# Kernel optimization log

Measured on AMD Instinct MI355X. Metric: run time of the kernel, lower is better.

Reference implementation:

```python
import jax, jax.numpy as jnp
import numpy as np

MAX_LEN, BATCH, EMB = 512, 32, 41
HID, UNITS = 800, 20
BOND_LENS = jnp.array([1.329, 1.459, 1.525], jnp.float32)
BOND_ANGLES = jnp.array([2.034, 2.119, 1.937], jnp.float32)
INIT_ABC = jnp.array([[0.0, 0.0, 1.0], [0.0, 1.0, 0.0], [1.0, 0.0, 0.0]], jnp.float32)


def _lstm_dir(x, w_ih, w_hh, b, reverse):
    # x: [T, B, in]; returns hidden states [T, B, H]
    T, B, _ = x.shape
    H = w_hh.shape[1]
    xs = jnp.flip(x, 0) if reverse else x
    xw = jnp.einsum('tbi,gi->tbg', xs, w_ih) + b  # precompute input projection

    def step(carry, xt):
        h, c = carry
        gates = xt + h @ w_hh.T
        i, f, g, o = jnp.split(gates, 4, axis=-1)
        c = jax.nn.sigmoid(f) * c + jax.nn.sigmoid(i) * jnp.tanh(g)
        h = jax.nn.sigmoid(o) * jnp.tanh(c)
        return (h, c), h

    init = (jnp.zeros((B, H), x.dtype), jnp.zeros((B, H), x.dtype))
    _, hs = jax.lax.scan(step, init, xw)
    return jnp.flip(hs, 0) if reverse else hs


def _bilstm_layer(x, w_ih, w_hh, b):
    # w_ih: [2, 4H, in]; w_hh: [2, 4H, H]; b: [2, 4H]
    fwd = _lstm_dir(x, w_ih[0], w_hh[0], b[0], False)
    bwd = _lstm_dir(x, w_ih[1], w_hh[1], b[1], True)
    return jnp.concatenate([fwd, bwd], axis=-1)


def _geometric_unit(coords3, triplet):
    # coords3: [3, B, 3] last three atoms; triplet: [B, 3] torsion angles
    A, Bc, C = coords3[0], coords3[1], coords3[2]
    new = []
    for i in range(3):
        Tang, R, P = BOND_ANGLES[i], BOND_LENS[i], triplet[:, i]
        D2 = jnp.stack([-R * jnp.cos(Tang) * jnp.ones_like(P),
                        R * jnp.cos(P) * jnp.sin(Tang),
                        R * jnp.sin(P) * jnp.sin(Tang)], axis=1)  # [B,3]
        BC = C - Bc
        bc = BC / jnp.linalg.norm(BC, axis=1, keepdims=True)
        AB = Bc - A
        N = jnp.cross(AB, bc)
        n = N / jnp.linalg.norm(N, axis=1, keepdims=True)
        M = jnp.stack([bc, jnp.cross(n, bc), n], axis=2)  # [B,3,3]
        D = jnp.einsum('bij,bj->bi', M, D2) + C
        A, Bc, C = Bc, C, D
        new.append(D)
    return jnp.stack([A, Bc, C]), jnp.stack(new)  # carry, [3,B,3]


def setup_inputs() -> dict:
    key = jax.random.key(0)
    ks = jax.random.split(key, 10)
    k = 1.0 / np.sqrt(HID)
    u = lambda kk, shp, lim: jax.random.uniform(kk, shp, jnp.float32, -lim, lim)
    in0, in1 = EMB + 1, 2 * HID
    return {
        'sequences': jax.random.normal(ks[0], (MAX_LEN, BATCH, EMB), jnp.float32),
        'lengths': jnp.full((BATCH,), MAX_LEN, jnp.int64 if jax.config.jax_enable_x64 else jnp.int32),
        'w_ih0': u(ks[1], (2, 4 * HID, in0), k),
        'w_hh0': u(ks[2], (2, 4 * HID, HID), k),
        'b0': u(ks[3], (2, 4 * HID), k),
        'w_ih1': u(ks[4], (2, 4 * HID, in1), k),
        'w_hh1': u(ks[5], (2, 4 * HID, HID), k),
        'b1': u(ks[6], (2, 4 * HID), k),
        'lin_w': u(ks[7], (UNITS, 2 * HID), 1.0 / np.sqrt(2 * HID)),
        'lin_b': u(ks[8], (UNITS,), 1.0 / np.sqrt(2 * HID)),
        'alphabet': jax.random.uniform(ks[9], (UNITS, 3), jnp.float32, -3.14, 3.14),
    }


def reference(sequences, lengths, w_ih0, w_hh0, b0, w_ih1, w_hh1, b1, lin_w, lin_b, alphabet):
    T, B, _ = sequences.shape
    abs_pos = jnp.broadcast_to(jnp.arange(T, dtype=sequences.dtype)[:, None, None], (T, B, 1))
    x = jnp.concatenate([sequences, abs_pos], axis=2)  # [T, B, EMB+1]
    # 2-layer bidirectional LSTM (all lengths == max_len -> packing is identity)
    h = _bilstm_layer(x, w_ih0, w_hh0, b0)
    h = _bilstm_layer(h, w_ih1, w_hh1, b1)  # [T, B, 2H]
    # linear -> softmax over alphabet, trig angle decode
    soft = jax.nn.softmax(h @ lin_w.T + lin_b, axis=2)  # [T, B, UNITS]
    sine = soft @ jnp.sin(alphabet)   # [T, B, 3]
    cosine = soft @ jnp.cos(alphabet)
    out = jnp.arctan2(sine, cosine)   # torsion angle triplets
    # sequential geometric coordinate recurrence over timesteps 1..T-1
    init = jnp.broadcast_to(INIT_ABC[:, None, :], (3, B, 3))
    _, new_coords = jax.lax.scan(_geometric_unit, init, out[1:])  # [T-1, 3, B, 3]
    pred_coords = jnp.concatenate([init, new_coords.reshape(-1, B, 3)], axis=0)
    return pred_coords  # [3 + 3*(T-1), B, 3]
```

## Files before the change

kernel.cpp:

```cpp
#include <hip/hip_runtime.h>
#include <math.h>

#define T_LEN 512
#define NB    32
#define EMB_  41
#define IN0_  42
#define HID_  800
#define G4_   3200
#define IN1_  1600
#define NU    20
#define NCH0  50
#define NCH   100

typedef unsigned short u16;
typedef unsigned int   u32;
typedef unsigned long long u64;
typedef __attribute__((ext_vector_type(8))) short short8;
typedef __attribute__((ext_vector_type(4))) float f32x4;

__device__ __forceinline__ float bf2f(u16 v) {
    union { u32 u; float f; } c; c.u = ((u32)v) << 16; return c.f;
}
__device__ __forceinline__ u16 f2bf(float f) {
    union { float f; u32 u; } c; c.f = f;
    u32 r = (c.u + 0x7fffu + ((c.u >> 16) & 1u)) >> 16;
    return (u16)r;
}
__device__ __forceinline__ short cvt_hl(float v, int hl) {
    u16 hi = f2bf(v);
    return hl ? (short)f2bf(v - bf2f(hi)) : (short)hi;
}
__device__ __forceinline__ f32x4 mfma16(short8 a, short8 b, f32x4 c) {
    return __builtin_amdgcn_mfma_f32_16x16x32_bf16(a, b, c, 0, 0, 0);
}
__device__ __forceinline__ void astore(u64* p, u64 v) {
    __hip_atomic_store(p, v, __ATOMIC_RELAXED, __HIP_MEMORY_SCOPE_AGENT);
}
__device__ __forceinline__ int afload(const int* p) {
    return __hip_atomic_load(p, __ATOMIC_RELAXED, __HIP_MEMORY_SCOPE_AGENT);
}
__device__ __forceinline__ void afstore(int* p, int v) {
    __hip_atomic_store(p, v, __ATOMIC_RELAXED, __HIP_MEMORY_SCOPE_AGENT);
}


__global__ __launch_bounds__(256, 1)
void lstm0_persist(const float* __restrict__ seq, const float* __restrict__ wih0,
                   const float* __restrict__ whh0, const float* __restrict__ bias,
                   u16* __restrict__ h0f, int* __restrict__ flags)
{
    __shared__ __align__(16) float part[4096];
    __shared__ __align__(16) u16 stageB[25600];
    __shared__ __align__(16) float w0l[64*48];
    __shared__ __align__(16) float xsl[2][32*48];
    __shared__ u16 hpk[2][NB*8];
    const int tid = threadIdx.x;
    const int d = blockIdx.x / NCH0, ch = blockIdx.x % NCH0;
    const int w = tid >> 6, l = tid & 63;
    const int p = w & 1, hl = w >> 1;
    int* myflags = flags + d*128;

    short8 wreg[2][25];
    {
        const int m = l & 15, g = p*2 + (m>>3);
#pragma unroll
        for (int T = 0; T < 2; ++T) {
            const int j = (ch*2 + T)*8 + (m&7);
            const float* base = whh0 + ((size_t)(d*G4_ + g*HID_ + j))*HID_ + (l>>4)*8;
#pragma unroll
            for (int kc = 0; kc < 25; ++kc) {
                float4 f0 = *(const float4*)(base + kc*32);
                float4 f1 = *(const float4*)(base + kc*32 + 4);
                short8 v;
                v[0]=cvt_hl(f0.x,hl); v[1]=cvt_hl(f0.y,hl); v[2]=cvt_hl(f0.z,hl); v[3]=cvt_hl(f0.w,hl);
                v[4]=cvt_hl(f1.x,hl); v[5]=cvt_hl(f1.y,hl); v[6]=cvt_hl(f1.z,hl); v[7]=cvt_hl(f1.w,hl);
                wreg[T][kc] = v;
            }
        }
    }
    for (int idx = tid; idx < 64*EMB_; idx += 256) {
        int r = idx / EMB_, k = idx % EMB_;
        int ju_ = r >> 2, g = r & 3;
        w0l[r*48 + k] = wih0[((size_t)(d*G4_ + g*HID_ + ch*16 + ju_))*IN0_ + k];
    }
    const int ju = tid >> 5, b = tid & 31;
    const int nt = b >> 4, n = b & 15;
    float biasr[2][4], wpos[2][4];
#pragma unroll
    for (int T = 0; T < 2; ++T) {
        const int j = ch*16 + T*8 + ju;
#pragma unroll
        for (int g = 0; g < 4; ++g) {
            biasr[T][g] = bias[d*G4_ + g*HID_ + j];
            wpos[T][g]  = wih0[((size_t)(d*G4_ + g*HID_ + j))*IN0_ + EMB_];
        }
    }
    float creg[2] = {0.f, 0.f};
    __syncthreads();

    for (int s = 0; s < T_LEN; ++s) {
        const int t = d ? (T_LEN-1-s) : s;

        for (int idx = tid; idx < 32*EMB_; idx += 256)
            xsl[s&1][(idx/EMB_)*48 + idx%EMB_] = seq[(size_t)t*(NB*EMB_) + idx];

        if (s > 0 && tid < NCH0)
            while (afload(myflags + tid) < s) __builtin_amdgcn_s_sleep(1);
        __syncthreads();

        if (s == 0) {
#pragma unroll
            for (int q = 0; q < 25; ++q) ((u64*)stageB)[tid + q*256] = 0ull;
        } else {
            const int tprev = d ? (T_LEN - s) : (s - 1);
            const u64* src = (const u64*)(h0f + (size_t)tprev*51200) + d*6400;
            u64 tmp[25];
#pragma unroll
            for (int q = 0; q < 25; ++q) tmp[q] = src[tid + q*256];
#pragma unroll
            for (int q = 0; q < 25; ++q) ((u64*)stageB)[tid + q*256] = tmp[q];
        }
        __syncthreads();

        f32x4 a00 = {0.f,0.f,0.f,0.f}, a01 = {0.f,0.f,0.f,0.f};
        f32x4 a10 = {0.f,0.f,0.f,0.f}, a11 = {0.f,0.f,0.f,0.f};
#pragma unroll
        for (int kc = 0; kc < 25; ++kc) {
            short8 b0 = *(const short8*)(stageB + kc*1024 + l*8);
            short8 b1 = *(const short8*)(stageB + kc*1024 + 512 + l*8);
            a00 = mfma16(wreg[0][kc], b0, a00);
            a01 = mfma16(wreg[0][kc], b1, a01);
            a10 = mfma16(wreg[1][kc], b0, a10);
            a11 = mfma16(wreg[1][kc], b1, a11);
        }
        {
            const int mrow = (l>>4)*4, nn = l & 15;
#pragma unroll
            for (int r = 0; r < 4; ++r) {
                part[((0*8 + (p*2+hl)*2 + 0)*16 + mrow + r)*16 + nn] = a00[r];
                part[((0*8 + (p*2+hl)*2 + 1)*16 + mrow + r)*16 + nn] = a01[r];
                part[((1*8 + (p*2+hl)*2 + 0)*16 + mrow + r)*16 + nn] = a10[r];
                part[((1*8 + (p*2+hl)*2 + 1)*16 + mrow + r)*16 + nn] = a11[r];
            }
        }
        __syncthreads();

#pragma unroll
        for (int T = 0; T < 2; ++T) {
            float dot0 = 0.f, dot1 = 0.f, dot2 = 0.f, dot3 = 0.f;
            const float* wr = &w0l[(T*8 + ju)*4*48];
            const float* xr = &xsl[s&1][b*48];
#pragma unroll
            for (int k4 = 0; k4 < 40; k4 += 4) {
                float4 xk = *(const float4*)(xr + k4);
                float4 w0 = *(const float4*)(wr + 0*48 + k4);
                float4 w1 = *(const float4*)(wr + 1*48 + k4);
                float4 w2 = *(const float4*)(wr + 2*48 + k4);
                float4 w3 = *(const float4*)(wr + 3*48 + k4);
                dot0 += w0.x*xk.x + w0.y*xk.y + w0.z*xk.z + w0.w*xk.w;
                dot1 += w1.x*xk.x + w1.y*xk.y + w1.z*xk.z + w1.w*xk.w;
                dot2 += w2.x*xk.x + w2.y*xk.y + w2.z*xk.z + w2.w*xk.w;
                dot3 += w3.x*xk.x + w3.y*xk.y + w3.z*xk.z + w3.w*xk.w;
            }
            float xk = xr[40];
            dot0 += wr[0*48+40]*xk; dot1 += wr[1*48+40]*xk;
            dot2 += wr[2*48+40]*xk; dot3 += wr[3*48+40]*xk;
            float v[4] = {dot0, dot1, dot2, dot3};
#pragma unroll
            for (int g = 0; g < 4; ++g) {
                const int pp = g >> 1, m = (g & 1)*8 + ju;
                v[g] += part[((T*8 + (pp*2+0)*2 + nt)*16 + m)*16 + n]
                      + part[((T*8 + (pp*2+1)*2 + nt)*16 + m)*16 + n]
                      + biasr[T][g] + (float)t * wpos[T][g];
            }
            float ig = 1.f/(1.f + expf(-v[0]));
            float fg = 1.f/(1.f + expf(-v[1]));
            float gg = tanhf(v[2]);
            float og = 1.f/(1.f + expf(-v[3]));
            creg[T] = fg * creg[T] + ig * gg;
            hpk[T][b*8 + ju] = f2bf(og * tanhf(creg[T]));
        }
        __syncthreads();

        if (tid < 128) {
            const int T = tid >> 6, tl = tid & 63;
            const int bb = tl >> 1, half = tl & 1;
            const u16* hp = &hpk[T][bb*8 + half*4];
            u64 pk = (u64)hp[0] | ((u64)hp[1]<<16) | ((u64)hp[2]<<32) | ((u64)hp[3]<<48);
            const int ch2 = ch*2 + T;
            const int ntb = bb >> 4, llb = ((ch2&3)<<4) | (bb&15);
            const int xoff = ((d*25 + (ch2>>2))*2 + ntb)*128 + llb*2 + half;
            astore((u64*)(h0f + (size_t)t*51200) + xoff, pk);
        }
        __syncthreads();
        if (tid == 0) afstore(myflags + ch, s+1);
    }
}

__global__ __launch_bounds__(256, 1)
void lstm1_persist(const float* __restrict__ wih1, const float* __restrict__ whh1,
                   const float* __restrict__ bias, const float* __restrict__ lin_w,
                   const u16* __restrict__ h0f, u16* __restrict__ h1f,
                   int* __restrict__ flags, float* __restrict__ logits)
{
    __shared__ __align__(16) u16 wihL[2*50*512];
    __shared__ __align__(16) u16 stageB[25600];
    __shared__ __align__(16) float part[2048];
    __shared__ u16 hpk[NB*8];
    const int tid = threadIdx.x;
    const int d = blockIdx.x / NCH, ch = blockIdx.x % NCH;
    const int w = tid >> 6, l = tid & 63;
    const int p = w & 1, hl = w >> 1;
    int* myflags = flags + d*128;

    short8 wreg[25];
    {
        const int m = l & 15, g = p*2 + (m>>3), j = ch*8 + (m&7);
        const float* base = whh1 + ((size_t)(d*G4_ + g*HID_ + j))*HID_ + (l>>4)*8;
#pragma unroll
        for (int kc = 0; kc < 25; ++kc) {
            float4 f0 = *(const float4*)(base + kc*32);
            float4 f1 = *(const float4*)(base + kc*32 + 4);
            short8 v;
            v[0]=cvt_hl(f0.x,hl); v[1]=cvt_hl(f0.y,hl); v[2]=cvt_hl(f0.z,hl); v[3]=cvt_hl(f0.w,hl);
            v[4]=cvt_hl(f1.x,hl); v[5]=cvt_hl(f1.y,hl); v[6]=cvt_hl(f1.z,hl); v[7]=cvt_hl(f1.w,hl);
            wreg[kc] = v;
        }
    }
    for (int o = tid; o < 6400; o += 256) {
        int pp = o / 3200, r = o % 3200, kc = r >> 6, ll = r & 63;
        int m = ll & 15, g = pp*2 + (m>>3), jj = ch*8 + (m&7);
        const float* base = wih1 + ((size_t)(d*G4_ + g*HID_ + jj))*IN1_ + kc*32 + (ll>>4)*8;
        float4 f0 = *(const float4*)base;
        float4 f1 = *(const float4*)(base + 4);
        short8 v;
        v[0]=(short)f2bf(f0.x); v[1]=(short)f2bf(f0.y); v[2]=(short)f2bf(f0.z); v[3]=(short)f2bf(f0.w);
        v[4]=(short)f2bf(f1.x); v[5]=(short)f2bf(f1.y); v[6]=(short)f2bf(f1.z); v[7]=(short)f2bf(f1.w);
        *(short8*)&wihL[o*8] = v;
    }
    const int ol = tid >> 5, ln = tid & 31;
    const int lo = ch*7 + ol;
    const bool lown = (ol < 7) && (lo < NB*NU);
    int lofs = 0;
    float wlin[25];
    if (lown) {
        const int bb = lo / NU, uu = lo % NU;
        lofs = (bb >> 4)*512 + ((((ln >> 3) << 4) | (bb & 15)))*8 + (ln & 7);
        const float* wrow = lin_w + (size_t)uu*IN1_ + d*HID_ + ln;
#pragma unroll
        for (int i = 0; i < 25; ++i) wlin[i] = wrow[i*32];
    }
    const int ju = tid >> 5, b = tid & 31;
    const int j = ch*8 + ju;
    const int nt = b >> 4, n = b & 15;
    float biasr[4];
#pragma unroll
    for (int g = 0; g < 4; ++g) biasr[g] = bias[d*G4_ + g*HID_ + j];
    float creg = 0.f;
    __syncthreads();

    for (int s = 0; s < T_LEN; ++s) {
        const int t = d ? (T_LEN-1-s) : s;

        f32x4 acc0 = {0.f,0.f,0.f,0.f}, acc1 = {0.f,0.f,0.f,0.f};
        {
            const u16* xb = h0f + (size_t)t*51200;
#pragma unroll 5
            for (int kc = 0; kc < 25; ++kc) {
                const int idx = hl*25 + kc;
                short8 a  = *(const short8*)&wihL[(p*50 + idx)*512 + l*8];
                short8 b0 = *(const short8*)(xb + idx*1024 + l*8);
                short8 b1 = *(const short8*)(xb + idx*1024 + 512 + l*8);
                acc0 = mfma16(a, b0, acc0);
                acc1 = mfma16(a, b1, acc1);
            }
        }

        if (s > 0 && tid < NCH)
            while (afload(myflags + tid) < s) __builtin_amdgcn_s_sleep(1);
        __syncthreads();

        if (s == 0) {
#pragma unroll
            for (int q = 0; q < 25; ++q) ((u64*)stageB)[tid + q*256] = 0ull;
        } else {
            const int tprev = d ? (T_LEN - s) : (s - 1);
            const u64* src = (const u64*)(h1f + (size_t)tprev*51200) + d*6400;
            u64 tmp[25];
#pragma unroll
            for (int q = 0; q < 25; ++q) tmp[q] = src[tid + q*256];
#pragma unroll
            for (int q = 0; q < 25; ++q) ((u64*)stageB)[tid + q*256] = tmp[q];
        }
        __syncthreads();

#pragma unroll 5
        for (int kc = 0; kc < 25; ++kc) {
            short8 b0 = *(const short8*)(stageB + kc*1024 + l*8);
            short8 b1 = *(const short8*)(stageB + kc*1024 + 512 + l*8);
            acc0 = mfma16(wreg[kc], b0, acc0);
            acc1 = mfma16(wreg[kc], b1, acc1);
        }
        {
            const int mrow = (l>>4)*4, nn = l & 15;
#pragma unroll
            for (int r = 0; r < 4; ++r) {
                part[(((p*2+hl)*2 + 0)*16 + mrow + r)*16 + nn] = acc0[r];
                part[(((p*2+hl)*2 + 1)*16 + mrow + r)*16 + nn] = acc1[r];
            }
        }
        __syncthreads();

        float v[4];
#pragma unroll
        for (int g = 0; g < 4; ++g) {
            const int pp = g >> 1, m = (g & 1)*8 + ju;
            v[g] = part[(((pp*2+0)*2 + nt)*16 + m)*16 + n]
                 + part[(((pp*2+1)*2 + nt)*16 + m)*16 + n] + biasr[g];
        }
        float ig = 1.f/(1.f + expf(-v[0]));
        float fg = 1.f/(1.f + expf(-v[1]));
        float gg = tanhf(v[2]);
        float og = 1.f/(1.f + expf(-v[3]));
        creg = fg * creg + ig * gg;
        float hn = og * tanhf(creg);
        hpk[b*8 + ju] = f2bf(hn);
        __syncthreads();

        if (tid < 64) {
            const int bb = tid >> 1, half = tid & 1;
            const u16* hp = &hpk[bb*8 + half*4];
            u64 pk = (u64)hp[0] | ((u64)hp[1]<<16) | ((u64)hp[2]<<32) | ((u64)hp[3]<<48);
            const int ntb = bb >> 4, llb = ((ch&3)<<4) | (bb&15);
            const int xoff = ((d*25 + (ch>>2))*2 + ntb)*128 + llb*2 + half;
            astore((u64*)(h1f + (size_t)t*51200) + xoff, pk);
        }
        __syncthreads();
        if (tid == 0) afstore(myflags + ch, s+1);

        if (s > 0 && lown) {
            float sum = 0.f;
#pragma unroll
            for (int i = 0; i < 25; ++i)
                sum += bf2f(stageB[i*1024 + lofs]) * wlin[i];
#pragma unroll
            for (int off2 = 16; off2; off2 >>= 1) sum += __shfl_down(sum, off2, 32);
            if (ln == 0) {
                const int tprev = d ? (T_LEN - s) : (s - 1);
                logits[((size_t)d*T_LEN + tprev)*640 + lo] = sum;
            }
        }
    }
    if (tid < NCH)
        while (afload(myflags + tid) < T_LEN) __builtin_amdgcn_s_sleep(1);
    __syncthreads();
    {
        const int tlast = d ? 0 : (T_LEN - 1);
        const u64* src = (const u64*)(h1f + (size_t)tlast*51200) + d*6400;
        u64 tmp[25];
#pragma unroll
        for (int q = 0; q < 25; ++q) tmp[q] = src[tid + q*256];
#pragma unroll
        for (int q = 0; q < 25; ++q) ((u64*)stageB)[tid + q*256] = tmp[q];
    }
    __syncthreads();
    if (lown) {
        float sum = 0.f;
#pragma unroll
        for (int i = 0; i < 25; ++i)
            sum += bf2f(stageB[i*1024 + lofs]) * wlin[i];
#pragma unroll
        for (int off2 = 16; off2; off2 >>= 1) sum += __shfl_down(sum, off2, 32);
        if (ln == 0) {
            const int tprev = d ? 0 : (T_LEN - 1);
            logits[((size_t)d*T_LEN + tprev)*640 + lo] = sum;
        }
    }
}

__global__ __launch_bounds__(256)
void epilogue(const float* __restrict__ logits, const float* __restrict__ lin_b,
              const float* __restrict__ alphabet, float* __restrict__ cs)
{
    __shared__ float sa[NU*3], ca[NU*3], lb[NU];
    const int tid = threadIdx.x;
    if (tid < NU*3) { float al = alphabet[tid]; sa[tid] = sinf(al); ca[tid] = cosf(al); }
    if (tid < NU) lb[tid] = lin_b[tid];
    __syncthreads();
    const int row = blockIdx.x*256 + tid;
    if (row >= T_LEN*NB) return;
    const int t = row >> 5, b = row & 31;
    float lg[NU];
    float m = -1e30f;
#pragma unroll 4
    for (int u = 0; u < NU; ++u) {
        lg[u] = lb[u] + logits[(size_t)t*640 + b*NU + u]
                      + logits[((size_t)T_LEN + t)*640 + b*NU + u];
        m = fmaxf(m, lg[u]);
    }
    float ssum = 0.f;
#pragma unroll 4
    for (int u = 0; u < NU; ++u) { lg[u] = expf(lg[u] - m); ssum += lg[u]; }
    float inv = 1.f / ssum;
#pragma unroll
    for (int i = 0; i < 3; ++i) {
        float sv = 0.f, cv = 0.f;
#pragma unroll 4
        for (int u = 0; u < NU; ++u) {
            float sw = lg[u] * inv;
            sv += sw * sa[u*3 + i];
            cv += sw * ca[u*3 + i];
        }
        float rinv = rsqrtf(fmaxf(sv*sv + cv*cv, 1e-30f));
        *(float2*)(cs + ((size_t)row*3 + i)*2) = make_float2(cv*rinv, sv*rinv);
    }
}

__global__ __launch_bounds__(64)
void geometry(const float* __restrict__ cs, float* __restrict__ out)
{
    const int b = threadIdx.x;
    if (b >= NB) return;
    const float blen[3] = {1.329f, 1.459f, 1.525f};
    const float bang[3] = {2.034f, 2.119f, 1.937f};
    float sT[3], cT[3];
#pragma unroll
    for (int i = 0; i < 3; ++i) { sT[i] = sinf(bang[i]); cT[i] = cosf(bang[i]); }

    float Ax=0.f,Ay=0.f,Az=1.f, Bx=0.f,By=1.f,Bz=0.f, Cx=1.f,Cy=0.f,Cz=0.f;
    out[(0*NB + b)*3 + 0] = 0.f; out[(0*NB + b)*3 + 1] = 0.f; out[(0*NB + b)*3 + 2] = 1.f;
    out[(1*NB + b)*3 + 0] = 0.f; out[(1*NB + b)*3 + 1] = 1.f; out[(1*NB + b)*3 + 2] = 0.f;
    out[(2*NB + b)*3 + 0] = 1.f; out[(2*NB + b)*3 + 1] = 0.f; out[(2*NB + b)*3 + 2] = 0.f;

    for (int t = 1; t < T_LEN; ++t) {
        float2 pc[3];
#pragma unroll
        for (int i = 0; i < 3; ++i)
            pc[i] = *(const float2*)(cs + (((size_t)t*NB + b)*3 + i)*2);
#pragma unroll
        for (int i = 0; i < 3; ++i) {
            float R = blen[i];
            float d2x = -R*cT[i], d2y = R*pc[i].x*sT[i], d2z = R*pc[i].y*sT[i];
            float bcx = Cx-Bx, bcy = Cy-By, bcz = Cz-Bz;
            float inv = rsqrtf(bcx*bcx + bcy*bcy + bcz*bcz);
            bcx *= inv; bcy *= inv; bcz *= inv;
            float abx = Bx-Ax, aby = By-Ay, abz = Bz-Az;
            float nx = aby*bcz - abz*bcy;
            float ny = abz*bcx - abx*bcz;
            float nz = abx*bcy - aby*bcx;
            inv = rsqrtf(fmaxf(nx*nx + ny*ny + nz*nz, 1e-30f));
            nx *= inv; ny *= inv; nz *= inv;
            float mx = ny*bcz - nz*bcy;
            float my = nz*bcx - nx*bcz;
            float mz = nx*bcy - ny*bcx;
            float Dx = bcx*d2x + mx*d2y + nx*d2z + Cx;
            float Dy = bcy*d2x + my*d2y + ny*d2z + Cy;
            float Dz = bcz*d2x + mz*d2y + nz*d2z + Cz;
            Ax=Bx; Ay=By; Az=Bz; Bx=Cx; By=Cy; Bz=Cz; Cx=Dx; Cy=Dy; Cz=Dz;
            const int r = 3 + (t-1)*3 + i;
            out[((size_t)r*NB + b)*3 + 0] = Dx;
            out[((size_t)r*NB + b)*3 + 1] = Dy;
            out[((size_t)r*NB + b)*3 + 2] = Dz;
        }
    }
}

extern "C" void kernel_launch(void* const* d_in, const int* in_sizes, int n_in,
                              void* d_out, int out_size, void* d_ws, size_t ws_size,
                              hipStream_t stream)
{
    (void)in_sizes; (void)n_in; (void)out_size; (void)ws_size;
    const float* seq   = (const float*)d_in[0];
    const float* w_ih0 = (const float*)d_in[2];
    const float* w_hh0 = (const float*)d_in[3];
    const float* b0    = (const float*)d_in[4];
    const float* w_ih1 = (const float*)d_in[5];
    const float* w_hh1 = (const float*)d_in[6];
    const float* b1    = (const float*)d_in[7];
    const float* lin_w = (const float*)d_in[8];
    const float* lin_b = (const float*)d_in[9];
    const float* alpha = (const float*)d_in[10];

    char* ws = (char*)d_ws;
    size_t off = 0;
    u16* h0f   = (u16*)(ws + off); off += 52428800ull;
    u16* h1f   = (u16*)(ws + off); off += 52428800ull;
    int* flagsL0 = (int*)(ws + off); off += 1024ull;
    int* flagsL1 = (int*)(ws + off); off += 1024ull;
    float* logits = (float*)(ws + off); off += 2621440ull;
    float* cs = (float*)(ws + off); off += 393216ull;

    hipMemsetAsync(flagsL0, 0, 2048, stream);

    lstm0_persist<<<dim3(2*NCH0), dim3(256), 0, stream>>>(seq, w_ih0, w_hh0, b0, h0f, flagsL0);

    lstm1_persist<<<dim3(2*NCH), dim3(256), 0, stream>>>(w_ih1, w_hh1, b1, lin_w, h0f, h1f,
                                                         flagsL1, logits);

    epilogue<<<dim3(64), dim3(256), 0, stream>>>(logits, lin_b, alpha, cs);
    geometry<<<dim3(1), dim3(64), 0, stream>>>(cs, (float*)d_out);
}
```

Baseline: 9.321 ms.

## Offload layer-1 input projection to producer blocks pipelined ahead of recurrence

Adds 50 producer blocks to the layer-1 persistent kernel. They compute the input projection (W_ih·h0) for 4 channel groups each and write the results into an XR-deep ring buffer in global memory. Flags and acks run the producers ahead of the 200 recurrent blocks, so the input GEMM comes off the recurrence's per-step critical path. The bf16 conversion of W_ih moves to a separate init kernel, and the h1 history shrinks to a 4-slot ring. The cost is extra global traffic, more inter-block synchronisation, and reliance on all 250 blocks being co-resident.

```diff
diff --git a/kernel.cpp b/kernel.cpp
--- a/kernel.cpp
+++ b/kernel.cpp
@@ -11,6 +11,8 @@
 #define NU    20
 #define NCH0  50
 #define NCH   100
+#define XR    8
+#define RH1   4
 
 typedef unsigned short u16;
 typedef unsigned int   u32;
@@ -36,6 +38,9 @@
 __device__ __forceinline__ void astore(u64* p, u64 v) {
     __hip_atomic_store(p, v, __ATOMIC_RELAXED, __HIP_MEMORY_SCOPE_AGENT);
 }
+__device__ __forceinline__ u64 aload(const u64* p) {
+    return __hip_atomic_load(p, __ATOMIC_RELAXED, __HIP_MEMORY_SCOPE_AGENT);
+}
 __device__ __forceinline__ int afload(const int* p) {
     return __hip_atomic_load(p, __ATOMIC_RELAXED, __HIP_MEMORY_SCOPE_AGENT);
 }
@@ -43,6 +48,27 @@
     __hip_atomic_store(p, v, __ATOMIC_RELAXED, __HIP_MEMORY_SCOPE_AGENT);
 }
 
+
+__global__ __launch_bounds__(256)
+void wihb_init(const float* __restrict__ wih1, u16* __restrict__ wihB)
+{
+    int gid = blockIdx.x*256 + threadIdx.x;
+    if (gid >= 2*100*2*50*64) return;
+    int u = gid;
+    const int l = u & 63; u >>= 6;
+    const int idx = u % 50; u /= 50;
+    const int p = u & 1; u >>= 1;
+    const int ch = u % 100; u /= 100;
+    const int dd = u;
+    const int m = l & 15, g = p*2 + (m>>3), j = ch*8 + (m&7);
+    const float* base = wih1 + ((size_t)(dd*G4_ + g*HID_ + j))*IN1_ + idx*32 + (l>>4)*8;
+    float4 f0 = *(const float4*)base;
+    float4 f1 = *(const float4*)(base + 4);
+    short8 v;
+    v[0]=(short)f2bf(f0.x); v[1]=(short)f2bf(f0.y); v[2]=(short)f2bf(f0.z); v[3]=(short)f2bf(f0.w);
+    v[4]=(short)f2bf(f1.x); v[5]=(short)f2bf(f1.y); v[6]=(short)f2bf(f1.z); v[7]=(short)f2bf(f1.w);
+    *(short8*)&wihB[(size_t)gid*8] = v;
+}
 
 __global__ __launch_bounds__(256, 1)
 void lstm0_persist(const float* __restrict__ seq, const float* __restrict__ wih0,
@@ -198,20 +224,73 @@
 }
 
 __global__ __launch_bounds__(256, 1)
-void lstm1_persist(const float* __restrict__ wih1, const float* __restrict__ whh1,
-                   const float* __restrict__ bias, const float* __restrict__ lin_w,
-                   const u16* __restrict__ h0f, u16* __restrict__ h1f,
-                   int* __restrict__ flags, float* __restrict__ logits)
+void lstm1_persist(const float* __restrict__ whh1, const float* __restrict__ bias,
+                   const float* __restrict__ lin_w, const u16* __restrict__ h0f,
+                   const u16* __restrict__ wihB, u16* __restrict__ h1f,
+                   float* __restrict__ xwf, int* __restrict__ flags,
+                   int* __restrict__ xwflag, int* __restrict__ ackf,
+                   float* __restrict__ logits)
 {
-    __shared__ __align__(16) u16 wihL[2*50*512];
     __shared__ __align__(16) u16 stageB[25600];
     __shared__ __align__(16) float part[2048];
     __shared__ u16 hpk[NB*8];
     const int tid = threadIdx.x;
-    const int d = blockIdx.x / NCH, ch = blockIdx.x % NCH;
     const int w = tid >> 6, l = tid & 63;
     const int p = w & 1, hl = w >> 1;
+
+    if (blockIdx.x >= 200) {
+        const int q = blockIdx.x - 200;
+        const int dq = q / 25, gq = q % 25;
+        int* acks = ackf + dq*100 + gq*4;
+        const u16* wb = wihB + ((size_t)(dq*100 + gq*4)*2)*50*512;
+        u64* dst = (u64*)xwf;
+
+        for (int s = 0; s < T_LEN; ++s) {
+            const int t = dq ? (T_LEN-1-s) : s;
+            if (s >= XR && tid < 4)
+                while (afload(acks + tid) < s - XR + 1) __builtin_amdgcn_s_sleep(1);
+            __syncthreads();
+
+            const u16* xb = h0f + (size_t)t*51200;
+            f32x4 ac0[4], ac1[4];
+#pragma unroll
+            for (int c = 0; c < 4; ++c) {
+                ac0[c] = (f32x4){0.f,0.f,0.f,0.f};
+                ac1[c] = (f32x4){0.f,0.f,0.f,0.f};
+            }
+#pragma unroll 5
+            for (int kc = 0; kc < 25; ++kc) {
+                const int idx = hl*25 + kc;
+                short8 b0 = *(const short8*)(xb + idx*1024 + l*8);
+                short8 b1 = *(const short8*)(xb + idx*1024 + 512 + l*8);
+#pragma unroll
+                for (int c = 0; c < 4; ++c) {
+                    short8 a = *(const short8*)(wb + (((size_t)c*2 + p)*50 + idx)*512 + l*8);
+                    ac0[c] = mfma16(a, b0, ac0[c]);
+                    ac1[c] = mfma16(a, b1, ac1[c]);
+                }
+            }
+#pragma unroll
+            for (int c = 0; c < 4; ++c) {
+                const size_t chg = (size_t)dq*100 + gq*4 + c;
+                size_t o0 = ((((((size_t)(s&(XR-1))*200 + chg)*2 + p)*2 + hl)*2 + 0)*64 + l)*2;
+                union { f32x4 v; u64 qq[2]; } c0, c1;
+                c0.v = ac0[c]; c1.v = ac1[c];
+                astore(dst + o0,       c0.qq[0]);
+                astore(dst + o0 + 1,   c0.qq[1]);
+                astore(dst + o0 + 128, c1.qq[0]);
+                astore(dst + o0 + 129, c1.qq[1]);
+            }
+            __syncthreads();
+            if (tid == 0) afstore(xwflag + q, s+1);
+        }
+        return;
+    }
+
+    const int d = blockIdx.x / NCH, ch = blockIdx.x % NCH;
     int* myflags = flags + d*128;
+    int* myack   = ackf + d*100 + ch;
+    const int myxwf = d*25 + (ch>>2);
 
     short8 wreg[25];
     {
@@ -226,17 +305,6 @@
             v[4]=cvt_hl(f1.x,hl); v[5]=cvt_hl(f1.y,hl); v[6]=cvt_hl(f1.z,hl); v[7]=cvt_hl(f1.w,hl);
             wreg[kc] = v;
         }
-    }
-    for (int o = tid; o < 6400; o += 256) {
-        int pp = o / 3200, r = o % 3200, kc = r >> 6, ll = r & 63;
-        int m = ll & 15, g = pp*2 + (m>>3), jj = ch*8 + (m&7);
-        const float* base = wih1 + ((size_t)(d*G4_ + g*HID_ + jj))*IN1_ + kc*32 + (ll>>4)*8;
-        float4 f0 = *(const float4*)base;
-        float4 f1 = *(const float4*)(base + 4);
-        short8 v;
-        v[0]=(short)f2bf(f0.x); v[1]=(short)f2bf(f0.y); v[2]=(short)f2bf(f0.z); v[3]=(short)f2bf(f0.w);
-        v[4]=(short)f2bf(f1.x); v[5]=(short)f2bf(f1.y); v[6]=(short)f2bf(f1.z); v[7]=(short)f2bf(f1.w);
-        *(short8*)&wihL[o*8] = v;
     }
     const int ol = tid >> 5, ln = tid & 31;
     const int lo = ch*7 + ol;
@@ -260,40 +328,37 @@
     __syncthreads();
 
     for (int s = 0; s < T_LEN; ++s) {
-        const int t = d ? (T_LEN-1-s) : s;
-
-        f32x4 acc0 = {0.f,0.f,0.f,0.f}, acc1 = {0.f,0.f,0.f,0.f};
-        {
-            const u16* xb = h0f + (size_t)t*51200;
-#pragma unroll 5
-            for (int kc = 0; kc < 25; ++kc) {
-                const int idx = hl*25 + kc;
-                short8 a  = *(const short8*)&wihL[(p*50 + idx)*512 + l*8];
-                short8 b0 = *(const short8*)(xb + idx*1024 + l*8);
-                short8 b1 = *(const short8*)(xb + idx*1024 + 512 + l*8);
-                acc0 = mfma16(a, b0, acc0);
-                acc1 = mfma16(a, b1, acc1);
-            }
-        }
-
         if (s > 0 && tid < NCH)
             while (afload(myflags + tid) < s) __builtin_amdgcn_s_sleep(1);
-        __syncthreads();
+        if (tid == 128)
+            while (afload(xwflag + myxwf) < s+1) __builtin_amdgcn_s_sleep(1);
+        __syncthreads();
+
+        const u64* xwp = (const u64*)xwf +
+            ((((((size_t)(s&(XR-1))*200 + d*100+ch)*2 + p)*2 + hl)*2 + 0)*64 + l)*2;
+        u64 xq0 = aload(xwp), xq1 = aload(xwp + 1);
+        u64 xq2 = aload(xwp + 128), xq3 = aload(xwp + 129);
 
         if (s == 0) {
 #pragma unroll
             for (int q = 0; q < 25; ++q) ((u64*)stageB)[tid + q*256] = 0ull;
         } else {
-            const int tprev = d ? (T_LEN - s) : (s - 1);
-            const u64* src = (const u64*)(h1f + (size_t)tprev*51200) + d*6400;
+            const u64* src = (const u64*)(h1f + (size_t)((s-1)&(RH1-1))*51200) + d*6400;
             u64 tmp[25];
 #pragma unroll
-            for (int q = 0; q < 25; ++q) tmp[q] = src[tid + q*256];
+            for (int q = 0; q < 25; ++q) tmp[q] = aload(src + tid + q*256);
 #pragma unroll
             for (int q = 0; q < 25; ++q) ((u64*)stageB)[tid + q*256] = tmp[q];
         }
         __syncthreads();
 
+        f32x4 acc0, acc1;
+        {
+            union { u64 qq[2]; f32x4 v; } c0, c1;
+            c0.qq[0] = xq0; c0.qq[1] = xq1;
+            c1.qq[0] = xq2; c1.qq[1] = xq3;
+            acc0 = c0.v; acc1 = c1.v;
+        }
 #pragma unroll 5
         for (int kc = 0; kc < 25; ++kc) {
             short8 b0 = *(const short8*)(stageB + kc*1024 + l*8);
@@ -333,10 +398,13 @@
             u64 pk = (u64)hp[0] | ((u64)hp[1]<<16) | ((u64)hp[2]<<32) | ((u64)hp[3]<<48);
             const int ntb = bb >> 4, llb = ((ch&3)<<4) | (bb&15);
             const int xoff = ((d*25 + (ch>>2))*2 + ntb)*128 + llb*2 + half;
-            astore((u64*)(h1f + (size_t)t*51200) + xoff, pk);
-        }
-        __syncthreads();
-        if (tid == 0) afstore(myflags + ch, s+1);
+            astore((u64*)(h1f + (size_t)(s&(RH1-1))*51200) + xoff, pk);
+        }
+        __syncthreads();
+        if (tid == 0) {
+            afstore(myflags + ch, s+1);
+            afstore(myack, s+1);
+        }
 
         if (s > 0 && lown) {
             float sum = 0.f;
@@ -355,11 +423,10 @@
         while (afload(myflags + tid) < T_LEN) __builtin_amdgcn_s_sleep(1);
     __syncthreads();
     {
-        const int tlast = d ? 0 : (T_LEN - 1);
-        const u64* src = (const u64*)(h1f + (size_t)tlast*51200) + d*6400;
+        const u64* src = (const u64*)(h1f + (size_t)((T_LEN-1)&(RH1-1))*51200) + d*6400;
         u64 tmp[25];
 #pragma unroll
-        for (int q = 0; q < 25; ++q) tmp[q] = src[tid + q*256];
+        for (int q = 0; q < 25; ++q) tmp[q] = aload(src + tid + q*256);
 #pragma unroll
         for (int q = 0; q < 25; ++q) ((u64*)stageB)[tid + q*256] = tmp[q];
     }
@@ -483,19 +550,25 @@
 
     char* ws = (char*)d_ws;
     size_t off = 0;
-    u16* h0f   = (u16*)(ws + off); off += 52428800ull;
-    u16* h1f   = (u16*)(ws + off); off += 52428800ull;
+    u16* h0f    = (u16*)(ws + off); off += 52428800ull;
+    u16* wihB   = (u16*)(ws + off); off += 20480000ull;
+    u16* h1f    = (u16*)(ws + off); off += (size_t)RH1*102400ull;
+    float* xwf  = (float*)(ws + off); off += (size_t)XR*200*8192ull;
     int* flagsL0 = (int*)(ws + off); off += 1024ull;
     int* flagsL1 = (int*)(ws + off); off += 1024ull;
+    int* xwflag  = (int*)(ws + off); off += 512ull;
+    int* ackf    = (int*)(ws + off); off += 1024ull;
     float* logits = (float*)(ws + off); off += 2621440ull;
     float* cs = (float*)(ws + off); off += 393216ull;
 
-    hipMemsetAsync(flagsL0, 0, 2048, stream);
+    hipMemsetAsync(flagsL0, 0, 1024 + 1024 + 512 + 1024, stream);
+
+    wihb_init<<<dim3(5000), dim3(256), 0, stream>>>(w_ih1, wihB);
 
     lstm0_persist<<<dim3(2*NCH0), dim3(256), 0, stream>>>(seq, w_ih0, w_hh0, b0, h0f, flagsL0);
 
-    lstm1_persist<<<dim3(2*NCH), dim3(256), 0, stream>>>(w_ih1, w_hh1, b1, lin_w, h0f, h1f,
-                                                         flagsL1, logits);
+    lstm1_persist<<<dim3(250), dim3(256), 0, stream>>>(w_hh1, b1, lin_w, h0f, wihB, h1f,
+                                                       xwf, flagsL1, xwflag, ackf, logits);
 
     epilogue<<<dim3(64), dim3(256), 0, stream>>>(logits, lin_b, alpha, cs);
     geometry<<<dim3(1), dim3(64), 0, stream>>>(cs, (float*)d_out);
```

Result: slower. 13.73 ms (+47.3%).

## Warp-specialize layer-1 LSTM: prefetch next-step input projection with extra waves

Applied to the files above, without the earlier changes.

Doubles the layer-1 persistent block to 512 threads. Four waves run the recurrent h@W_hh matmul and gate update, while four new waves compute the next timestep's input projection from W_ih (pre-converted to bf16 in global memory by a new init kernel) into a double-buffered LDS slot. The logits dot product also moves to the producer waves. This takes the input-projection MFMA work and the logits work off the serial recurrent critical path. In exchange, W_ih is now streamed from global or L2 every step instead of held in LDS, a conversion kernel and a larger workspace are added, and there are more barriers per step.

```diff
diff --git a/kernel.cpp b/kernel.cpp
--- a/kernel.cpp
+++ b/kernel.cpp
@@ -43,6 +43,27 @@
     __hip_atomic_store(p, v, __ATOMIC_RELAXED, __HIP_MEMORY_SCOPE_AGENT);
 }
 
+
+__global__ __launch_bounds__(256)
+void wihb_init(const float* __restrict__ wih1, u16* __restrict__ wihB)
+{
+    int gid = blockIdx.x*256 + threadIdx.x;
+    if (gid >= 2*100*2*50*64) return;
+    int u = gid;
+    const int l = u & 63; u >>= 6;
+    const int idx = u % 50; u /= 50;
+    const int p = u & 1; u >>= 1;
+    const int ch = u % 100; u /= 100;
+    const int dd = u;
+    const int m = l & 15, g = p*2 + (m>>3), j = ch*8 + (m&7);
+    const float* base = wih1 + ((size_t)(dd*G4_ + g*HID_ + j))*IN1_ + idx*32 + (l>>4)*8;
+    float4 f0 = *(const float4*)base;
+    float4 f1 = *(const float4*)(base + 4);
+    short8 v;
+    v[0]=(short)f2bf(f0.x); v[1]=(short)f2bf(f0.y); v[2]=(short)f2bf(f0.z); v[3]=(short)f2bf(f0.w);
+    v[4]=(short)f2bf(f1.x); v[5]=(short)f2bf(f1.y); v[6]=(short)f2bf(f1.z); v[7]=(short)f2bf(f1.w);
+    *(short8*)&wihB[(size_t)gid*8] = v;
+}
 
 __global__ __launch_bounds__(256, 1)
 void lstm0_persist(const float* __restrict__ seq, const float* __restrict__ wih0,
@@ -197,24 +218,27 @@
     }
 }
 
-__global__ __launch_bounds__(256, 1)
-void lstm1_persist(const float* __restrict__ wih1, const float* __restrict__ whh1,
-                   const float* __restrict__ bias, const float* __restrict__ lin_w,
-                   const u16* __restrict__ h0f, u16* __restrict__ h1f,
+__global__ __launch_bounds__(512, 2)
+void lstm1_persist(const float* __restrict__ whh1, const float* __restrict__ bias,
+                   const float* __restrict__ lin_w, const u16* __restrict__ h0f,
+                   const u16* __restrict__ wihB, u16* __restrict__ h1f,
                    int* __restrict__ flags, float* __restrict__ logits)
 {
-    __shared__ __align__(16) u16 wihL[2*50*512];
     __shared__ __align__(16) u16 stageB[25600];
     __shared__ __align__(16) float part[2048];
+    __shared__ __align__(16) float xwr[2][2048];
     __shared__ u16 hpk[NB*8];
     const int tid = threadIdx.x;
     const int d = blockIdx.x / NCH, ch = blockIdx.x % NCH;
     const int w = tid >> 6, l = tid & 63;
-    const int p = w & 1, hl = w >> 1;
+    const bool comp = w < 4;
+    const int p = w & 1, hl = (w >> 1) & 1;
+    const int xw_ = w - 4;
+    const int xp = xw_ & 1, xhl = (xw_ >> 1) & 1;
     int* myflags = flags + d*128;
 
     short8 wreg[25];
-    {
+    if (comp) {
         const int m = l & 15, g = p*2 + (m>>3), j = ch*8 + (m&7);
         const float* base = whh1 + ((size_t)(d*G4_ + g*HID_ + j))*HID_ + (l>>4)*8;
 #pragma unroll
@@ -227,20 +251,12 @@
             wreg[kc] = v;
         }
     }
-    for (int o = tid; o < 6400; o += 256) {
-        int pp = o / 3200, r = o % 3200, kc = r >> 6, ll = r & 63;
-        int m = ll & 15, g = pp*2 + (m>>3), jj = ch*8 + (m&7);
-        const float* base = wih1 + ((size_t)(d*G4_ + g*HID_ + jj))*IN1_ + kc*32 + (ll>>4)*8;
-        float4 f0 = *(const float4*)base;
-        float4 f1 = *(const float4*)(base + 4);
-        short8 v;
-        v[0]=(short)f2bf(f0.x); v[1]=(short)f2bf(f0.y); v[2]=(short)f2bf(f0.z); v[3]=(short)f2bf(f0.w);
-        v[4]=(short)f2bf(f1.x); v[5]=(short)f2bf(f1.y); v[6]=(short)f2bf(f1.z); v[7]=(short)f2bf(f1.w);
-        *(short8*)&wihL[o*8] = v;
-    }
-    const int ol = tid >> 5, ln = tid & 31;
+    const u16* wb = wihB + ((size_t)((d*100 + ch)*2 + xp)*50)*512;
+
+    const int xt = tid & 255;
+    const int ol = xt >> 5, ln = xt & 31;
     const int lo = ch*7 + ol;
-    const bool lown = (ol < 7) && (lo < NB*NU);
+    const bool lown = (!comp) && (ol < 7) && (lo < NB*NU);
     int lofs = 0;
     float wlin[25];
     if (lown) {
@@ -251,80 +267,117 @@
         for (int i = 0; i < 25; ++i) wlin[i] = wrow[i*32];
     }
     const int ju = tid >> 5, b = tid & 31;
-    const int j = ch*8 + ju;
     const int nt = b >> 4, n = b & 15;
     float biasr[4];
-#pragma unroll
-    for (int g = 0; g < 4; ++g) biasr[g] = bias[d*G4_ + g*HID_ + j];
+    if (comp) {
+        const int j = ch*8 + ju;
+#pragma unroll
+        for (int g = 0; g < 4; ++g) biasr[g] = bias[d*G4_ + g*HID_ + j];
+    }
     float creg = 0.f;
     __syncthreads();
 
+    if (!comp) {
+        const int t0 = d ? (T_LEN-1) : 0;
+        const u16* xb = h0f + (size_t)t0*51200;
+        f32x4 a0 = {0.f,0.f,0.f,0.f}, a1 = {0.f,0.f,0.f,0.f};
+#pragma unroll 5
+        for (int kc = 0; kc < 25; ++kc) {
+            const int idx = xhl*25 + kc;
+            short8 a  = *(const short8*)(wb + idx*512 + l*8);
+            short8 b0 = *(const short8*)(xb + idx*1024 + l*8);
+            short8 b1 = *(const short8*)(xb + idx*1024 + 512 + l*8);
+            a0 = mfma16(a, b0, a0);
+            a1 = mfma16(a, b1, a1);
+        }
+        *(f32x4*)&xwr[0][((xp*2+xhl)*2 + 0)*256 + l*4] = a0;
+        *(f32x4*)&xwr[0][((xp*2+xhl)*2 + 1)*256 + l*4] = a1;
+    }
+    __syncthreads();
+
     for (int s = 0; s < T_LEN; ++s) {
         const int t = d ? (T_LEN-1-s) : s;
 
-        f32x4 acc0 = {0.f,0.f,0.f,0.f}, acc1 = {0.f,0.f,0.f,0.f};
-        {
-            const u16* xb = h0f + (size_t)t*51200;
+        if (comp && s > 0 && tid < NCH)
+            while (afload(myflags + tid) < s) __builtin_amdgcn_s_sleep(1);
+        __syncthreads();
+
+        if (comp) {
+            if (s == 0) {
+#pragma unroll
+                for (int q = 0; q < 25; ++q) ((u64*)stageB)[tid + q*256] = 0ull;
+            } else {
+                const int tprev = d ? (T_LEN - s) : (s - 1);
+                const u64* src = (const u64*)(h1f + (size_t)tprev*51200) + d*6400;
+                u64 tmp[25];
+#pragma unroll
+                for (int q = 0; q < 25; ++q) tmp[q] = src[tid + q*256];
+#pragma unroll
+                for (int q = 0; q < 25; ++q) ((u64*)stageB)[tid + q*256] = tmp[q];
+            }
+        } else if (s + 1 < T_LEN) {
+            const int t1 = d ? (T_LEN-1-(s+1)) : (s+1);
+            const u16* xb = h0f + (size_t)t1*51200;
+            f32x4 a0 = {0.f,0.f,0.f,0.f}, a1 = {0.f,0.f,0.f,0.f};
 #pragma unroll 5
             for (int kc = 0; kc < 25; ++kc) {
-                const int idx = hl*25 + kc;
-                short8 a  = *(const short8*)&wihL[(p*50 + idx)*512 + l*8];
+                const int idx = xhl*25 + kc;
+                short8 a  = *(const short8*)(wb + idx*512 + l*8);
                 short8 b0 = *(const short8*)(xb + idx*1024 + l*8);
                 short8 b1 = *(const short8*)(xb + idx*1024 + 512 + l*8);
-                acc0 = mfma16(a, b0, acc0);
-                acc1 = mfma16(a, b1, acc1);
-            }
-        }
-
-        if (s > 0 && tid < NCH)
-            while (afload(myflags + tid) < s) __builtin_amdgcn_s_sleep(1);
-        __syncthreads();
-
-        if (s == 0) {
-#pragma unroll
-            for (int q = 0; q < 25; ++q) ((u64*)stageB)[tid + q*256] = 0ull;
-        } else {
-            const int tprev = d ? (T_LEN - s) : (s - 1);
-            const u64* src = (const u64*)(h1f + (size_t)tprev*51200) + d*6400;
-            u64 tmp[25];
-#pragma unroll
-            for (int q = 0; q < 25; ++q) tmp[q] = src[tid + q*256];
-#pragma unroll
-            for (int q = 0; q < 25; ++q) ((u64*)stageB)[tid + q*256] = tmp[q];
-        }
-        __syncthreads();
-
+                a0 = mfma16(a, b0, a0);
+                a1 = mfma16(a, b1, a1);
+            }
+            *(f32x4*)&xwr[(s+1)&1][((xp*2+xhl)*2 + 0)*256 + l*4] = a0;
+            *(f32x4*)&xwr[(s+1)&1][((xp*2+xhl)*2 + 1)*256 + l*4] = a1;
+        }
+        __syncthreads();
+
+        if (comp) {
+            f32x4 acc0 = *(const f32x4*)&xwr[s&1][((p*2+hl)*2 + 0)*256 + l*4];
+            f32x4 acc1 = *(const f32x4*)&xwr[s&1][((p*2+hl)*2 + 1)*256 + l*4];
 #pragma unroll 5
-        for (int kc = 0; kc < 25; ++kc) {
-            short8 b0 = *(const short8*)(stageB + kc*1024 + l*8);
-            short8 b1 = *(const short8*)(stageB + kc*1024 + 512 + l*8);
-            acc0 = mfma16(wreg[kc], b0, acc0);
-            acc1 = mfma16(wreg[kc], b1, acc1);
-        }
-        {
+            for (int kc = 0; kc < 25; ++kc) {
+                short8 b0 = *(const short8*)(stageB + kc*1024 + l*8);
+                short8 b1 = *(const short8*)(stageB + kc*1024 + 512 + l*8);
+                acc0 = mfma16(wreg[kc], b0, acc0);
+                acc1 = mfma16(wreg[kc], b1, acc1);
+            }
             const int mrow = (l>>4)*4, nn = l & 15;
 #pragma unroll
             for (int r = 0; r < 4; ++r) {
                 part[(((p*2+hl)*2 + 0)*16 + mrow + r)*16 + nn] = acc0[r];
                 part[(((p*2+hl)*2 + 1)*16 + mrow + r)*16 + nn] = acc1[r];
             }
-        }
-        __syncthreads();
-
-        float v[4];
-#pragma unroll
-        for (int g = 0; g < 4; ++g) {
-            const int pp = g >> 1, m = (g & 1)*8 + ju;
-            v[g] = part[(((pp*2+0)*2 + nt)*16 + m)*16 + n]
-                 + part[(((pp*2+1)*2 + nt)*16 + m)*16 + n] + biasr[g];
-        }
-        float ig = 1.f/(1.f + expf(-v[0]));
-        float fg = 1.f/(1.f + expf(-v[1]));
-        float gg = tanhf(v[2]);
-        float og = 1.f/(1.f + expf(-v[3]));
-        creg = fg * creg + ig * gg;
-        float hn = og * tanhf(creg);
-        hpk[b*8 + ju] = f2bf(hn);
+        } else if (s > 0 && lown) {
+            float sum = 0.f;
+#pragma unroll
+            for (int i = 0; i < 25; ++i)
+                sum += bf2f(stageB[i*1024 + lofs]) * wlin[i];
+#pragma unroll
+            for (int off2 = 16; off2; off2 >>= 1) sum += __shfl_down(sum, off2, 32);
+            if (ln == 0) {
+                const int tprev = d ? (T_LEN - s) : (s - 1);
+                logits[((size_t)d*T_LEN + tprev)*640 + lo] = sum;
+            }
+        }
+        __syncthreads();
+
+        if (comp) {
+            float v[4];
+#pragma unroll
+            for (int g = 0; g < 4; ++g) {
+                const int pp = g >> 1, m = (g & 1)*8 + ju;
+                v[g] = part[(((pp*2+0)*2 + nt)*16 + m)*16 + n]
+                     + part[(((pp*2+1)*2 + nt)*16 + m)*16 + n] + biasr[g];
+            }
+            float ig = 1.f/(1.f + expf(-v[0]));
+            float fg = 1.f/(1.f + expf(-v[1]));
+            float gg = tanhf(v[2]);
+            float og = 1.f/(1.f + expf(-v[3]));
+            creg = fg * creg + ig * gg;
+            hpk[b*8 + ju] = f2bf(og * tanhf(creg));
+        }
         __syncthreads();
 
         if (tid < 64) {
@@ -337,24 +390,11 @@
         }
         __syncthreads();
         if (tid == 0) afstore(myflags + ch, s+1);
-
-        if (s > 0 && lown) {
-            float sum = 0.f;
-#pragma unroll
-            for (int i = 0; i < 25; ++i)
-                sum += bf2f(stageB[i*1024 + lofs]) * wlin[i];
-#pragma unroll
-            for (int off2 = 16; off2; off2 >>= 1) sum += __shfl_down(sum, off2, 32);
-            if (ln == 0) {
-                const int tprev = d ? (T_LEN - s) : (s - 1);
-                logits[((size_t)d*T_LEN + tprev)*640 + lo] = sum;
-            }
-        }
     }
     if (tid < NCH)
         while (afload(myflags + tid) < T_LEN) __builtin_amdgcn_s_sleep(1);
     __syncthreads();
-    {
+    if (comp) {
         const int tlast = d ? 0 : (T_LEN - 1);
         const u64* src = (const u64*)(h1f + (size_t)tlast*51200) + d*6400;
         u64 tmp[25];
@@ -483,8 +523,9 @@
 
     char* ws = (char*)d_ws;
     size_t off = 0;
-    u16* h0f   = (u16*)(ws + off); off += 52428800ull;
-    u16* h1f   = (u16*)(ws + off); off += 52428800ull;
+    u16* h0f    = (u16*)(ws + off); off += 52428800ull;
+    u16* h1f    = (u16*)(ws + off); off += 52428800ull;
+    u16* wihB   = (u16*)(ws + off); off += 20480000ull;
     int* flagsL0 = (int*)(ws + off); off += 1024ull;
     int* flagsL1 = (int*)(ws + off); off += 1024ull;
     float* logits = (float*)(ws + off); off += 2621440ull;
@@ -492,9 +533,11 @@
 
     hipMemsetAsync(flagsL0, 0, 2048, stream);
 
+    wihb_init<<<dim3(5000), dim3(256), 0, stream>>>(w_ih1, wihB);
+
     lstm0_persist<<<dim3(2*NCH0), dim3(256), 0, stream>>>(seq, w_ih0, w_hh0, b0, h0f, flagsL0);
 
-    lstm1_persist<<<dim3(2*NCH), dim3(256), 0, stream>>>(w_ih1, w_hh1, b1, lin_w, h0f, h1f,
+    lstm1_persist<<<dim3(2*NCH), dim3(512), 0, stream>>>(w_hh1, b1, lin_w, h0f, wihB, h1f,
                                                          flagsL1, logits);
 
     epilogue<<<dim3(64), dim3(256), 0, stream>>>(logits, lin_b, alpha, cs);
```

After: 12.92 ms. 1.39x slower.

## Stage layer-1 input activations in LDS and stream pre-packed input weights from global

Applied to the files above, without the earlier changes.

The bf16 conversion and packing of the layer-1 input weights moves into a separate pre-kernel that writes them to workspace. The persistent kernel then reads its A-operand from that global (L2-resident) buffer instead of LDS. The freed LDS holds a per-step staging copy of the layer-0 output row, loaded cooperatively and overlapped with the recurrent-state load, so the MFMA B operands come from LDS rather than scattered global reads. The linear-head weights are also dropped from registers and read from global on each use, which lowers register pressure but adds global traffic and an extra kernel launch.

```diff
diff --git a/kernel.cpp b/kernel.cpp
--- a/kernel.cpp
+++ b/kernel.cpp
@@ -43,6 +43,27 @@
     __hip_atomic_store(p, v, __ATOMIC_RELAXED, __HIP_MEMORY_SCOPE_AGENT);
 }
 
+
+__global__ __launch_bounds__(256)
+void wihb_init(const float* __restrict__ wih1, u16* __restrict__ wihB)
+{
+    int gid = blockIdx.x*256 + threadIdx.x;
+    if (gid >= 2*100*2*50*64) return;
+    int u = gid;
+    const int l = u & 63; u >>= 6;
+    const int idx = u % 50; u /= 50;
+    const int p = u & 1; u >>= 1;
+    const int ch = u % 100; u /= 100;
+    const int dd = u;
+    const int m = l & 15, g = p*2 + (m>>3), j = ch*8 + (m&7);
+    const float* base = wih1 + ((size_t)(dd*G4_ + g*HID_ + j))*IN1_ + idx*32 + (l>>4)*8;
+    float4 f0 = *(const float4*)base;
+    float4 f1 = *(const float4*)(base + 4);
+    short8 v;
+    v[0]=(short)f2bf(f0.x); v[1]=(short)f2bf(f0.y); v[2]=(short)f2bf(f0.z); v[3]=(short)f2bf(f0.w);
+    v[4]=(short)f2bf(f1.x); v[5]=(short)f2bf(f1.y); v[6]=(short)f2bf(f1.z); v[7]=(short)f2bf(f1.w);
+    *(short8*)&wihB[(size_t)gid*8] = v;
+}
 
 __global__ __launch_bounds__(256, 1)
 void lstm0_persist(const float* __restrict__ seq, const float* __restrict__ wih0,
@@ -198,12 +219,12 @@
 }
 
 __global__ __launch_bounds__(256, 1)
-void lstm1_persist(const float* __restrict__ wih1, const float* __restrict__ whh1,
-                   const float* __restrict__ bias, const float* __restrict__ lin_w,
-                   const u16* __restrict__ h0f, u16* __restrict__ h1f,
+void lstm1_persist(const float* __restrict__ whh1, const float* __restrict__ bias,
+                   const float* __restrict__ lin_w, const u16* __restrict__ h0f,
+                   const u16* __restrict__ wihB, u16* __restrict__ h1f,
                    int* __restrict__ flags, float* __restrict__ logits)
 {
-    __shared__ __align__(16) u16 wihL[2*50*512];
+    __shared__ __align__(16) u16 xstage[51200];
     __shared__ __align__(16) u16 stageB[25600];
     __shared__ __align__(16) float part[2048];
     __shared__ u16 hpk[NB*8];
@@ -227,28 +248,17 @@
             wreg[kc] = v;
         }
     }
-    for (int o = tid; o < 6400; o += 256) {
-        int pp = o / 3200, r = o % 3200, kc = r >> 6, ll = r & 63;
-        int m = ll & 15, g = pp*2 + (m>>3), jj = ch*8 + (m&7);
-        const float* base = wih1 + ((size_t)(d*G4_ + g*HID_ + jj))*IN1_ + kc*32 + (ll>>4)*8;
-        float4 f0 = *(const float4*)base;
-        float4 f1 = *(const float4*)(base + 4);
-        short8 v;
-        v[0]=(short)f2bf(f0.x); v[1]=(short)f2bf(f0.y); v[2]=(short)f2bf(f0.z); v[3]=(short)f2bf(f0.w);
-        v[4]=(short)f2bf(f1.x); v[5]=(short)f2bf(f1.y); v[6]=(short)f2bf(f1.z); v[7]=(short)f2bf(f1.w);
-        *(short8*)&wihL[o*8] = v;
-    }
+    const u16* wb = wihB + ((size_t)((d*100 + ch)*2 + p)*50)*512;
+
     const int ol = tid >> 5, ln = tid & 31;
     const int lo = ch*7 + ol;
     const bool lown = (ol < 7) && (lo < NB*NU);
     int lofs = 0;
-    float wlin[25];
+    const float* wrow = lin_w;
     if (lown) {
         const int bb = lo / NU, uu = lo % NU;
         lofs = (bb >> 4)*512 + ((((ln >> 3) << 4) | (bb & 15)))*8 + (ln & 7);
-        const float* wrow = lin_w + (size_t)uu*IN1_ + d*HID_ + ln;
-#pragma unroll
-        for (int i = 0; i < 25; ++i) wlin[i] = wrow[i*32];
+        wrow = lin_w + (size_t)uu*IN1_ + d*HID_ + ln;
     }
     const int ju = tid >> 5, b = tid & 31;
     const int j = ch*8 + ju;
@@ -261,39 +271,48 @@
 
     for (int s = 0; s < T_LEN; ++s) {
         const int t = d ? (T_LEN-1-s) : s;
-
-        f32x4 acc0 = {0.f,0.f,0.f,0.f}, acc1 = {0.f,0.f,0.f,0.f};
-        {
-            const u16* xb = h0f + (size_t)t*51200;
-#pragma unroll 5
-            for (int kc = 0; kc < 25; ++kc) {
-                const int idx = hl*25 + kc;
-                short8 a  = *(const short8*)&wihL[(p*50 + idx)*512 + l*8];
-                short8 b0 = *(const short8*)(xb + idx*1024 + l*8);
-                short8 b1 = *(const short8*)(xb + idx*1024 + 512 + l*8);
-                acc0 = mfma16(a, b0, acc0);
-                acc1 = mfma16(a, b1, acc1);
-            }
-        }
+        const u64* xsrc = (const u64*)(h0f + (size_t)t*51200);
+
+        u64 xa[25];
+#pragma unroll
+        for (int q = 0; q < 25; ++q) xa[q] = xsrc[tid + q*256];
 
         if (s > 0 && tid < NCH)
             while (afload(myflags + tid) < s) __builtin_amdgcn_s_sleep(1);
         __syncthreads();
 
-        if (s == 0) {
-#pragma unroll
-            for (int q = 0; q < 25; ++q) ((u64*)stageB)[tid + q*256] = 0ull;
-        } else {
+        u64 st[25];
+        if (s > 0) {
             const int tprev = d ? (T_LEN - s) : (s - 1);
             const u64* src = (const u64*)(h1f + (size_t)tprev*51200) + d*6400;
-            u64 tmp[25];
-#pragma unroll
-            for (int q = 0; q < 25; ++q) tmp[q] = src[tid + q*256];
-#pragma unroll
-            for (int q = 0; q < 25; ++q) ((u64*)stageB)[tid + q*256] = tmp[q];
-        }
-        __syncthreads();
-
+#pragma unroll
+            for (int q = 0; q < 25; ++q) st[q] = src[tid + q*256];
+        }
+#pragma unroll
+        for (int q = 0; q < 25; ++q) ((u64*)xstage)[tid + q*256] = xa[q];
+#pragma unroll
+        for (int q = 0; q < 25; ++q) xa[q] = xsrc[tid + (25+q)*256];
+        if (s > 0) {
+#pragma unroll
+            for (int q = 0; q < 25; ++q) ((u64*)stageB)[tid + q*256] = st[q];
+        } else {
+#pragma unroll
+            for (int q = 0; q < 25; ++q) ((u64*)stageB)[tid + q*256] = 0ull;
+        }
+#pragma unroll
+        for (int q = 0; q < 25; ++q) ((u64*)xstage)[tid + (25+q)*256] = xa[q];
+        __syncthreads();
+
+        f32x4 acc0 = {0.f,0.f,0.f,0.f}, acc1 = {0.f,0.f,0.f,0.f};
+#pragma unroll 5
+        for (int kc = 0; kc < 25; ++kc) {
+            const int idx = hl*25 + kc;
+            short8 a  = *(const short8*)(wb + idx*512 + l*8);
+            short8 b0 = *(const short8*)(xstage + idx*1024 + l*8);
+            short8 b1 = *(const short8*)(xstage + idx*1024 + 512 + l*8);
+            acc0 = mfma16(a, b0, acc0);
+            acc1 = mfma16(a, b1, acc1);
+        }
 #pragma unroll 5
         for (int kc = 0; kc < 25; ++kc) {
             short8 b0 = *(const short8*)(stageB + kc*1024 + l*8);
@@ -342,7 +361,7 @@
             float sum = 0.f;
 #pragma unroll
             for (int i = 0; i < 25; ++i)
-                sum += bf2f(stageB[i*1024 + lofs]) * wlin[i];
+                sum += bf2f(stageB[i*1024 + lofs]) * wrow[i*32];
 #pragma unroll
             for (int off2 = 16; off2; off2 >>= 1) sum += __shfl_down(sum, off2, 32);
             if (ln == 0) {
@@ -368,7 +387,7 @@
         float sum = 0.f;
 #pragma unroll
         for (int i = 0; i < 25; ++i)
-            sum += bf2f(stageB[i*1024 + lofs]) * wlin[i];
+            sum += bf2f(stageB[i*1024 + lofs]) * wrow[i*32];
 #pragma unroll
         for (int off2 = 16; off2; off2 >>= 1) sum += __shfl_down(sum, off2, 32);
         if (ln == 0) {
@@ -483,8 +502,9 @@
 
     char* ws = (char*)d_ws;
     size_t off = 0;
-    u16* h0f   = (u16*)(ws + off); off += 52428800ull;
-    u16* h1f   = (u16*)(ws + off); off += 52428800ull;
+    u16* h0f    = (u16*)(ws + off); off += 52428800ull;
+    u16* h1f    = (u16*)(ws + off); off += 52428800ull;
+    u16* wihB   = (u16*)(ws + off); off += 20480000ull;
     int* flagsL0 = (int*)(ws + off); off += 1024ull;
     int* flagsL1 = (int*)(ws + off); off += 1024ull;
     float* logits = (float*)(ws + off); off += 2621440ull;
@@ -492,9 +512,11 @@
 
     hipMemsetAsync(flagsL0, 0, 2048, stream);
 
+    wihb_init<<<dim3(5000), dim3(256), 0, stream>>>(w_ih1, wihB);
+
     lstm0_persist<<<dim3(2*NCH0), dim3(256), 0, stream>>>(seq, w_ih0, w_hh0, b0, h0f, flagsL0);
 
-    lstm1_persist<<<dim3(2*NCH), dim3(256), 0, stream>>>(w_ih1, w_hh1, b1, lin_w, h0f, h1f,
+    lstm1_persist<<<dim3(2*NCH), dim3(256), 0, stream>>>(w_hh1, b1, lin_w, h0f, wihB, h1f,
                                                          flagsL1, logits);
 
     epilogue<<<dim3(64), dim3(256), 0, stream>>>(logits, lin_b, alpha, cs);
```

New measurement: 12.27 ms. 31.6% more time.
